# Kernel tuning notes

Hardware: AMD Instinct MI355X
Metric: run time of the kernel (lower is better)

The kernel has to match this reference:

```python
import jax, jax.numpy as jnp
import numpy as np
from jax import lax


def gru_cell(x, h, Wih, Whh, bih, bhh):
    # PyTorch GRU cell: gates ordered [r, z, n]
    gi = x @ Wih.T + bih            # [B, 3H]
    gh = h @ Whh.T + bhh            # [B, 3H]
    ir, iz, inn = jnp.split(gi, 3, axis=-1)
    hr, hz, hn = jnp.split(gh, 3, axis=-1)
    r = jax.nn.sigmoid(ir + hr)
    z = jax.nn.sigmoid(iz + hz)
    n = jnp.tanh(inn + r * hn)
    return (1.0 - z) * n + z * h


def setup_inputs() -> dict:
    key = jax.random.key(0)
    Vs = Vt = 32000; E = 256; H = 512; B = 32; S = 256; T = 64
    ks = jax.random.split(key, 32)

    def p(k, shape):
        return jax.random.normal(k, shape, dtype=jnp.float32) * 0.05

    return {
        "src": jax.random.randint(ks[0], (B, S), 0, Vs),
        "tgt": jax.random.randint(ks[1], (B, T), 0, Vt),
        "enc_emb": p(ks[2], (Vs, E)),
        "enc_Wih": p(ks[3], (3 * H, E)),
        "enc_Whh": p(ks[4], (3 * H, H)),
        "enc_bih": p(ks[5], (3 * H,)),
        "enc_bhh": p(ks[6], (3 * H,)),
        "dec_emb": p(ks[7], (Vt, E)),
        "attn_W1": p(ks[8], (H, H)),
        "attn_b1": p(ks[9], (H,)),
        "attn_W2": p(ks[10], (H, H)),
        "attn_b2": p(ks[11], (H,)),
        "attn_v": p(ks[12], (H,)),
        "dec_Wih": p(ks[13], (3 * H, E + H)),
        "dec_Whh": p(ks[14], (3 * H, H)),
        "dec_bih": p(ks[15], (3 * H,)),
        "dec_bhh": p(ks[16], (3 * H,)),
        "fc_W": p(ks[17], (Vt, H)),
        "fc_b": p(ks[18], (Vt,)),
    }


def reference(src, tgt, enc_emb, enc_Wih, enc_Whh, enc_bih, enc_bhh,
              dec_emb, attn_W1, attn_b1, attn_W2, attn_b2, attn_v,
              dec_Wih, dec_Whh, dec_bih, dec_bhh, fc_W, fc_b):
    B = src.shape[0]
    H = enc_Whh.shape[1]

    # ---- Encoder: GRU over src tokens ----
    src_e = enc_emb[src]                       # [B, S, E]

    def enc_step(h, x_t):
        h2 = gru_cell(x_t, h, enc_Wih, enc_Whh, enc_bih, enc_bhh)
        return h2, h2

    h0 = jnp.zeros((B, H), dtype=src_e.dtype)
    hT, enc_outs = lax.scan(enc_step, h0, src_e.transpose(1, 0, 2))
    enc_outs = enc_outs.transpose(1, 0, 2)     # [B, S, H]

    # Precompute encoder-side attention projection (loop-invariant)
    enc_proj = enc_outs @ attn_W2.T + attn_b2  # [B, S, H]

    # ---- Decoder: per-step Bahdanau attention + GRU + fc ----
    tgt_e = dec_emb[tgt].transpose(1, 0, 2)    # [T, B, E]

    def dec_step(h, x_t):
        q = jnp.tanh(enc_proj + (h @ attn_W1.T + attn_b1)[:, None, :])  # [B,S,H]
        scores = q @ attn_v                                             # [B,S]
        w = jax.nn.softmax(scores, axis=-1)
        ctx = jnp.einsum('bs,bsh->bh', w, enc_outs)                     # [B,H]
        rnn_in = jnp.concatenate([x_t, ctx], axis=-1)                   # [B,E+H]
        h2 = gru_cell(rnn_in, h, dec_Wih, dec_Whh, dec_bih, dec_bhh)
        logits = h2 @ fc_W.T + fc_b                                     # [B,V]
        return h2, logits

    _, outs = lax.scan(dec_step, hT, tgt_e)    # [T, B, V]
    return outs.transpose(1, 0, 2)             # [B, T, V]
```

## Files before the change

### kernel.cpp

```cpp
#include <hip/hip_runtime.h>
#include <hip/hip_bf16.h>
#include <stdint.h>

#define DEV __device__ __forceinline__
typedef unsigned short u16;
typedef unsigned int   u32;
typedef unsigned long long u64;

static constexpr int SS = 256;
static constexpr int TT = 64;
static constexpr int EE = 256;
static constexpr int HH = 512;
static constexpr int G3 = 1536;
static constexpr int VV = 32000;
static constexpr int HP  = 516;
static constexpr int WPE = 516;
static constexpr int WPD = 520;
static constexpr int CP8 = 520;

using frag   = __attribute__((ext_vector_type(8))) short;
using f32x4v = __attribute__((ext_vector_type(4))) float;

DEV float blo(u32 u){ union{u32 i; float f;} x; x.i = u << 16;         return x.f; }
DEV float bhi(u32 u){ union{u32 i; float f;} x; x.i = u & 0xffff0000u; return x.f; }
DEV float bf2f(u16 u){ union{u32 i; float f;} x; x.i = ((u32)u) << 16; return x.f; }
DEV u16 f2bf(float f){ union{float f; u32 u;} v; v.f = f;
  u32 r = v.u + 0x7fffu + ((v.u >> 16) & 1u); return (u16)(r >> 16); }
DEV float sigf (float x){ return 1.0f / (1.0f + __expf(-x)); }
DEV float tanh_(float x){ return 1.0f - 2.0f / (1.0f + __expf(2.0f * x)); }
DEV void unp8(float* d, uint4 u){
  d[0]=blo(u.x); d[1]=bhi(u.x); d[2]=blo(u.y); d[3]=bhi(u.y);
  d[4]=blo(u.z); d[5]=bhi(u.z); d[6]=blo(u.w); d[7]=bhi(u.w);
}
DEV float4 unp4(u64 v){
  return make_float4(bf2f((u16)v), bf2f((u16)(v >> 16)),
                     bf2f((u16)(v >> 32)), bf2f((u16)(v >> 48)));
}
DEV float dot4(float acc, float4 w, float4 x){
  acc = fmaf(w.x,x.x,acc); acc = fmaf(w.y,x.y,acc);
  acc = fmaf(w.z,x.z,acc); acc = fmaf(w.w,x.w,acc);
  return acc;
}
DEV float fma44(float acc, float4 w0, float4 w1, float4 h0, float4 h1){
  return dot4(dot4(acc, w0, h0), w1, h1);
}
DEV float fma8(float acc, const float* w, float4 a, float4 b){
  acc = fmaf(w[0],a.x,acc); acc = fmaf(w[1],a.y,acc);
  acc = fmaf(w[2],a.z,acc); acc = fmaf(w[3],a.w,acc);
  acc = fmaf(w[4],b.x,acc); acc = fmaf(w[5],b.y,acc);
  acc = fmaf(w[6],b.z,acc); acc = fmaf(w[7],b.w,acc);
  return acc;
}
DEV float fma8p(float acc, const float* w, const float* x){
  #pragma unroll
  for (int e = 0; e < 8; ++e) acc = fmaf(w[e], x[e], acc);
  return acc;
}

DEV void  ast_f(float* p, float v){ __hip_atomic_store(p, v, __ATOMIC_RELAXED, __HIP_MEMORY_SCOPE_AGENT); }
DEV void  ast_u(u32* p, u32 v)    { __hip_atomic_store(p, v, __ATOMIC_RELAXED, __HIP_MEMORY_SCOPE_AGENT); }
DEV float ald_f(const float* p)   { return __hip_atomic_load((float*)p, __ATOMIC_RELAXED, __HIP_MEMORY_SCOPE_AGENT); }
DEV u64   ald_u8(const u64* p)    { return __hip_atomic_load((u64*)p,   __ATOMIC_RELAXED, __HIP_MEMORY_SCOPE_AGENT); }
DEV u32   ald_u (const u32* p)    { return __hip_atomic_load((u32*)p,   __ATOMIC_RELAXED, __HIP_MEMORY_SCOPE_AGENT); }

DEV void grid_bar(u32* flags, int bid, int nb, u32 epoch){
  __syncthreads();
  if (threadIdx.x == 0) ast_u(&flags[bid * 32], epoch);
  if (threadIdx.x < (u32)nb) {
    while (ald_u(&flags[threadIdx.x * 32]) < epoch)
      __builtin_amdgcn_s_sleep(1);
  }
  __syncthreads();
}

__global__ __launch_bounds__(256)
void k_embed_gemm(const int* __restrict__ tok, int Tlen,
                  const float* __restrict__ emb,
                  const float* __restrict__ W, int wstride,
                  const float* __restrict__ bias,
                  u16* __restrict__ gi)
{
  __shared__ float es[16][EE];
  const int tid = threadIdx.x;
  const int r0 = blockIdx.y * 16;
  #pragma unroll
  for (int rr = 0; rr < 16; ++rr) {
    int r = r0 + rr;
    int token = tok[(r & 31) * Tlen + (r >> 5)];
    es[rr][tid] = emb[(size_t)token * EE + tid];
  }
  __syncthreads();
  const int jl = tid & 63;
  const int rg = (tid >> 6) << 2;
  const int jbase = blockIdx.x * 256 + jl;
  float acc[4][4];
  #pragma unroll
  for (int jj = 0; jj < 4; ++jj) {
    float bv = bias[jbase + jj * 64];
    #pragma unroll
    for (int rr = 0; rr < 4; ++rr) acc[jj][rr] = bv;
  }
  const float4* w0 = (const float4*)(W + (size_t)(jbase      ) * wstride);
  const float4* w1 = (const float4*)(W + (size_t)(jbase +  64) * wstride);
  const float4* w2 = (const float4*)(W + (size_t)(jbase + 128) * wstride);
  const float4* w3 = (const float4*)(W + (size_t)(jbase + 192) * wstride);
  for (int k4 = 0; k4 < EE / 4; ++k4) {
    float4 wv0 = w0[k4], wv1 = w1[k4], wv2 = w2[k4], wv3 = w3[k4];
    #pragma unroll
    for (int rr = 0; rr < 4; ++rr) {
      float4 e = *(const float4*)&es[rg + rr][k4 * 4];
      acc[0][rr] = dot4(acc[0][rr], wv0, e);
      acc[1][rr] = dot4(acc[1][rr], wv1, e);
      acc[2][rr] = dot4(acc[2][rr], wv2, e);
      acc[3][rr] = dot4(acc[3][rr], wv3, e);
    }
  }
  #pragma unroll
  for (int rr = 0; rr < 4; ++rr)
    #pragma unroll
    for (int jj = 0; jj < 4; ++jj)
      gi[(size_t)(r0 + rg + rr) * G3 + jbase + jj * 64] = f2bf(acc[jj][rr]);
}

__global__ __launch_bounds__(256)
void k_enc_scan(const u16* __restrict__ gi, const float* __restrict__ Whh,
                const float* __restrict__ bhh, u16* __restrict__ hring,
                u16* __restrict__ enc_outs, u32* __restrict__ flags)
{
  __shared__ float hs[32 * HP];
  __shared__ float wsl[12 * WPE];
  __shared__ float h2t[4][32];
  const int tid = threadIdx.x;
  const int bid = blockIdx.x;
  const int i0 = bid * 4;
  #pragma unroll
  for (int j = 0; j < 6; ++j) {
    int f = (j * 256 + tid) * 4;
    int rowl = f >> 9, k = f & 511;
    int g = rowl >> 2, ri = rowl & 3;
    *(float4*)&wsl[rowl * WPE + k] =
      *(const float4*)(Whh + (size_t)(g * 512 + i0 + ri) * 512 + k);
  }
  const int i_l = tid >> 6, lane = tid & 63, b = lane >> 1, kh = lane & 1;
  const int i = i0 + i_l;
  const float* w0 = wsl + (0 * 4 + i_l) * WPE + kh * 256;
  const float* w1 = wsl + (1 * 4 + i_l) * WPE + kh * 256;
  const float* w2 = wsl + (2 * 4 + i_l) * WPE + kh * 256;
  const float bR = bhh[i], bZ = bhh[i + 512], bN = bhh[i + 1024];
  for (int t = 0; t < SS; ++t) {
    const u64* hsrc = (const u64*)(hring + (size_t)t * 16384);
    #pragma unroll
    for (int j = 0; j < 16; ++j) {
      int idx = j * 256 + tid;
      u64 v = ald_u8(hsrc + idx);
      int bb = idx >> 7, m = (idx & 127) * 4;
      *(float4*)&hs[bb * HP + m] = unp4(v);
    }
    __syncthreads();
    float aR = 0.f, aZ = 0.f, aN = 0.f;
    const float* hb = hs + b * HP + kh * 256;
    for (int k8 = 0; k8 < 32; ++k8) {
      float4 h0 = *(const float4*)&hb[k8*8], h1 = *(const float4*)&hb[k8*8+4];
      aR = fma44(aR, *(const float4*)&w0[k8*8], *(const float4*)&w0[k8*8+4], h0, h1);
      aZ = fma44(aZ, *(const float4*)&w1[k8*8], *(const float4*)&w1[k8*8+4], h0, h1);
      aN = fma44(aN, *(const float4*)&w2[k8*8], *(const float4*)&w2[k8*8+4], h0, h1);
    }
    aR += __shfl_xor(aR, 1);
    aZ += __shfl_xor(aZ, 1);
    aN += __shfl_xor(aN, 1);
    if (kh == 0) {
      const size_t g = ((size_t)t * 32 + b) * G3;
      float r = sigf (bf2f(gi[g +        i]) + aR + bR);
      float z = sigf (bf2f(gi[g +  512 + i]) + aZ + bZ);
      float n = tanh_(bf2f(gi[g + 1024 + i]) + r * (aN + bN));
      float h2 = z * hs[b * HP + i] + (1.f - z) * n;
      enc_outs[((size_t)b * 256 + t) * 512 + i] = f2bf(h2);
      h2t[i_l][b] = h2;
    }
    __syncthreads();
    if (tid < 64) {
      int p = tid >> 5, bq = tid & 31;
      u32 pk = (u32)f2bf(h2t[2*p][bq]) | ((u32)f2bf(h2t[2*p+1][bq]) << 16);
      ast_u((u32*)(hring + (size_t)(t + 1) * 16384) + bq * 256 + bid * 2 + p, pk);
    }
    grid_bar(flags, bid, 128, (u32)(t + 1));
  }
}

__global__ __launch_bounds__(256)
void k_proj(const u16* __restrict__ A, const float* __restrict__ W,
            const float* __restrict__ bias, u16* __restrict__ Out)
{
  __shared__ float es[16][HH];
  const int tid = threadIdx.x;
  const int r0 = blockIdx.y * 16;
  #pragma unroll
  for (int j = 0; j < 4; ++j) {
    int u = j * 256 + tid;
    int row = u >> 6, k = (u & 63) * 8;
    float d[8]; unp8(d, *(const uint4*)(A + (size_t)(r0 + row) * HH + k));
    *(float4*)&es[row][k]     = make_float4(d[0],d[1],d[2],d[3]);
    *(float4*)&es[row][k + 4] = make_float4(d[4],d[5],d[6],d[7]);
  }
  __syncthreads();
  const int jl = tid & 63;
  const int rg = (tid >> 6) << 2;
  const int jbase = blockIdx.x * 256 + jl;
  float acc[4][4];
  #pragma unroll
  for (int jj = 0; jj < 4; ++jj) {
    float bv = bias[jbase + jj * 64];
    #pragma unroll
    for (int rr = 0; rr < 4; ++rr) acc[jj][rr] = bv;
  }
  const float4* w0 = (const float4*)(W + (size_t)(jbase      ) * HH);
  const float4* w1 = (const float4*)(W + (size_t)(jbase +  64) * HH);
  const float4* w2 = (const float4*)(W + (size_t)(jbase + 128) * HH);
  const float4* w3 = (const float4*)(W + (size_t)(jbase + 192) * HH);
  for (int k4 = 0; k4 < HH / 4; ++k4) {
    float4 wv0 = w0[k4], wv1 = w1[k4], wv2 = w2[k4], wv3 = w3[k4];
    #pragma unroll
    for (int rr = 0; rr < 4; ++rr) {
      float4 e = *(const float4*)&es[rg + rr][k4 * 4];
      acc[0][rr] = dot4(acc[0][rr], wv0, e);
      acc[1][rr] = dot4(acc[1][rr], wv1, e);
      acc[2][rr] = dot4(acc[2][rr], wv2, e);
      acc[3][rr] = dot4(acc[3][rr], wv3, e);
    }
  }
  #pragma unroll
  for (int rr = 0; rr < 4; ++rr)
    #pragma unroll
    for (int jj = 0; jj < 4; ++jj)
      Out[(size_t)(r0 + rg + rr) * HH + jbase + jj * 64] = f2bf(acc[jj][rr]);
}

__global__ __launch_bounds__(256)
void k_dec_scan(const u16* __restrict__ gi, u16* __restrict__ hring,
                const float* __restrict__ W1, const float* __restrict__ b1,
                const float* __restrict__ av,
                const u16* __restrict__ enc_proj, const u16* __restrict__ enc_outs,
                const float* __restrict__ Whh, const float* __restrict__ Wih,
                const float* __restrict__ bhh,
                float* __restrict__ aring, u16* __restrict__ ctxP,
                float* __restrict__ sringP, u16* __restrict__ h2bf,
                u32* __restrict__ flags)
{
  __shared__ float hs8[8 * HP];
  __shared__ u16  csb8[8 * CP8];
  __shared__ u16  wlds[112 * WPD];
  __shared__ float as_[512], vs_[512];
  __shared__ float scq[4][64], wts[64];
  __shared__ float rs[8];
  __shared__ float h2t[16][8];
  const int tid = threadIdx.x;
  const int bid = blockIdx.x;
  const int bg = bid >> 5, ig = bid & 31;
  const int b_l = tid >> 5, i_l = (tid >> 1) & 15, kh = tid & 1;
  const int i = ig * 16 + i_l;
  const int bglob = bg * 8 + b_l;
  const int pb = bid >> 2, sq = bid & 3;
  vs_[tid] = av[tid]; vs_[tid + 256] = av[tid + 256];
  for (int j = 0; j < 56; ++j) {
    int idx = j * 256 + tid;
    int row = idx >> 7, k4 = idx & 127;
    const float* src;
    if (row < 16)      src = W1  + (size_t)(ig * 16 + row) * 512 + k4 * 4;
    else if (row < 64) { int rr = row - 16; int g = rr >> 4, ii = rr & 15;
                         src = Whh + (size_t)(g * 512 + ig * 16 + ii) * 512 + k4 * 4; }
    else               { int rr = row - 64; int g = rr >> 4, ii = rr & 15;
                         src = Wih + (size_t)(g * 512 + ig * 16 + ii) * 768 + 256 + k4 * 4; }
    float4 w = *(const float4*)src;
    int f = row * WPD + k4 * 4;
    wlds[f] = f2bf(w.x); wlds[f+1] = f2bf(w.y); wlds[f+2] = f2bf(w.z); wlds[f+3] = f2bf(w.w);
  }
  const u16* w1r = wlds + (      i_l) * WPD + kh * 256;
  const u16* whr = wlds + (16  + i_l) * WPD + kh * 256;
  const u16* whz = wlds + (32  + i_l) * WPD + kh * 256;
  const u16* whn = wlds + (48  + i_l) * WPD + kh * 256;
  const u16* wir = wlds + (64  + i_l) * WPD + kh * 256;
  const u16* wiz = wlds + (80  + i_l) * WPD + kh * 256;
  const u16* win = wlds + (96  + i_l) * WPD + kh * 256;
  const float bR = bhh[i], bZ = bhh[i + 512], bN = bhh[i + 1024];
  const float b1i = b1[i];
  u32 ep = 0;
  for (int t = 0; t < TT; ++t) {
    const u64* hsrc = (const u64*)(hring + (size_t)(256 + t) * 16384);
    #pragma unroll
    for (int j = 0; j < 4; ++j) {
      int idx = j * 256 + tid;
      int lb = idx >> 7, gu = idx & 127;
      u64 v = ald_u8(hsrc + (size_t)(bg * 8 + lb) * 128 + gu);
      *(float4*)&hs8[lb * HP + gu * 4] = unp4(v);
    }
    __syncthreads();
    {
      const float* hb = hs8 + b_l * HP + kh * 256;
      float acc = 0.f;
      for (int k8 = 0; k8 < 32; ++k8) {
        float wf[8]; unp8(wf, *(const uint4*)(w1r + k8 * 8));
        acc = fma8(acc, wf, *(const float4*)&hb[k8*8], *(const float4*)&hb[k8*8+4]);
      }
      acc += __shfl_xor(acc, 1);
      if (kh == 0) ast_f(&aring[(size_t)t * 16384 + bglob * 512 + i], acc + b1i);
    }
    ++ep; grid_bar(flags, bid, 128, ep);
    {
      u64 v = ald_u8((const u64*)(aring + (size_t)t * 16384 + pb * 512) + tid);
      union { u64 q; float f[2]; } cv; cv.q = v;
      as_[2 * tid] = cv.f[0]; as_[2 * tid + 1] = cv.f[1];
    }
    __syncthreads();
    {
      const int kp = tid >> 6, s_l = tid & 63;
      const int s = sq * 64 + s_l;
      const u16* pr = enc_proj + ((size_t)pb * 256 + s) * 512 + kp * 128;
      const float* ak = as_ + kp * 128;
      const float* vk = vs_ + kp * 128;
      float acc = 0.f;
      for (int k8 = 0; k8 < 16; ++k8) {
        float d[8]; unp8(d, *(const uint4*)(pr + k8 * 8));
        #pragma unroll
        for (int e = 0; e < 8; ++e)
          acc += vk[k8 * 8 + e] * tanh_(d[e] + ak[k8 * 8 + e]);
      }
      scq[kp][s_l] = acc;
    }
    __syncthreads();
    if (tid < 64) {
      float sc = (scq[0][tid] + scq[1][tid]) + (scq[2][tid] + scq[3][tid]);
      float e = __expf(sc);
      wts[tid] = e;
      float su = e;
      #pragma unroll
      for (int d = 1; d < 64; d <<= 1) su += __shfl_xor(su, d);
      if (tid == 0) ast_f(&sringP[t * 128 + sq * 32 + pb], su);
    }
    __syncthreads();
    {
      const int k0 = tid * 2;
      float c0 = 0.f, c1 = 0.f;
      const u16* eo = enc_outs + ((size_t)pb * 256 + sq * 64) * 512 + k0;
      for (int s = 0; s < 64; ++s) {
        float w = wts[s];
        u32 pair = *(const u32*)(eo + (size_t)s * 512);
        c0 = fmaf(w, blo(pair), c0);
        c1 = fmaf(w, bhi(pair), c1);
      }
      u32 pk = (u32)f2bf(c0) | ((u32)f2bf(c1) << 16);
      ast_u((u32*)(ctxP + (size_t)t * 65536 + (sq * 32 + pb) * 512 + k0), pk);
    }
    ++ep; grid_bar(flags, bid, 128, ep);
    if (tid < 8) {
      const float* sp = sringP + t * 128;
      int bq = bg * 8 + tid;
      rs[tid] = 1.f / ((ald_f(sp + bq) + ald_f(sp + 32 + bq)) +
                       (ald_f(sp + 64 + bq) + ald_f(sp + 96 + bq)));
    }
    __syncthreads();
    #pragma unroll
    for (int j = 0; j < 4; ++j) {
      int idx = j * 256 + tid;
      int lb = idx >> 7, gu = idx & 127;
      const u64* bp = (const u64*)(ctxP + (size_t)t * 65536);
      float c[4] = {0,0,0,0};
      #pragma unroll
      for (int q = 0; q < 4; ++q) {
        float4 d = unp4(ald_u8(bp + (size_t)(q * 32 + bg * 8 + lb) * 128 + gu));
        c[0] += d.x; c[1] += d.y; c[2] += d.z; c[3] += d.w;
      }
      float r = rs[lb];
      int m = gu * 4;
      *(u32*)&csb8[lb * CP8 + m]     = (u32)f2bf(c[0]*r) | ((u32)f2bf(c[1]*r) << 16);
      *(u32*)&csb8[lb * CP8 + m + 2] = (u32)f2bf(c[2]*r) | ((u32)f2bf(c[3]*r) << 16);
    }
    __syncthreads();
    {
      const float* hb = hs8 + b_l * HP + kh * 256;
      const u16*   cb = csb8 + b_l * CP8 + kh * 256;
      float hR=0.f,hZ=0.f,hN=0.f,cR=0.f,cZ=0.f,cN=0.f;
      for (int k8 = 0; k8 < 32; ++k8) {
        float4 h0 = *(const float4*)&hb[k8*8], h1 = *(const float4*)&hb[k8*8+4];
        float cf[8]; unp8(cf, *(const uint4*)(cb + k8 * 8));
        float wf[8];
        unp8(wf, *(const uint4*)(whr + k8 * 8)); hR = fma8(hR, wf, h0, h1);
        unp8(wf, *(const uint4*)(whz + k8 * 8)); hZ = fma8(hZ, wf, h0, h1);
        unp8(wf, *(const uint4*)(whn + k8 * 8)); hN = fma8(hN, wf, h0, h1);
        unp8(wf, *(const uint4*)(wir + k8 * 8)); cR = fma8p(cR, wf, cf);
        unp8(wf, *(const uint4*)(wiz + k8 * 8)); cZ = fma8p(cZ, wf, cf);
        unp8(wf, *(const uint4*)(win + k8 * 8)); cN = fma8p(cN, wf, cf);
      }
      hR += __shfl_xor(hR, 1); hZ += __shfl_xor(hZ, 1); hN += __shfl_xor(hN, 1);
      cR += __shfl_xor(cR, 1); cZ += __shfl_xor(cZ, 1); cN += __shfl_xor(cN, 1);
      if (kh == 0) {
        const size_t g = ((size_t)t * 32 + bglob) * G3;
        float r = sigf (bf2f(gi[g +        i]) + cR + hR + bR);
        float z = sigf (bf2f(gi[g +  512 + i]) + cZ + hZ + bZ);
        float n = tanh_(bf2f(gi[g + 1024 + i]) + cN + r * (hN + bN));
        float h2 = z * hs8[b_l * HP + i] + (1.f - z) * n;
        h2bf[((size_t)t * 32 + bglob) * 512 + i] = f2bf(h2);
        h2t[i_l][b_l] = h2;
      }
    }
    __syncthreads();
    if (tid < 64) {
      int p = tid >> 3, bl = tid & 7;
      u32 pk = (u32)f2bf(h2t[2*p][bl]) | ((u32)f2bf(h2t[2*p+1][bl]) << 16);
      ast_u((u32*)(hring + (size_t)(257 + t) * 16384)
            + (bg * 8 + bl) * 256 + ig * 8 + p, pk);
    }
    ++ep; grid_bar(flags, bid, 128, ep);
  }
}

__global__ __launch_bounds__(256)
void k_cvt(const float* __restrict__ in, u16* __restrict__ out)
{
  size_t i = ((size_t)blockIdx.x * 256 + threadIdx.x) * 8;
  float4 a = *(const float4*)(in + i);
  float4 b = *(const float4*)(in + i + 4);
  union { uint4 v; u16 s[8]; } u;
  u.s[0]=f2bf(a.x); u.s[1]=f2bf(a.y); u.s[2]=f2bf(a.z); u.s[3]=f2bf(a.w);
  u.s[4]=f2bf(b.x); u.s[5]=f2bf(b.y); u.s[6]=f2bf(b.z); u.s[7]=f2bf(b.w);
  *(uint4*)(out + i) = u.v;
}

__global__ __launch_bounds__(256)
void k_logits_mfma(const u16* __restrict__ A, const u16* __restrict__ Wb,
                   const float* __restrict__ bias, float* __restrict__ out)
{
  __shared__ u16 Al[64 * 512];
  const int tid = threadIdx.x;
  const int r0 = blockIdx.x * 64;
  const int v0 = blockIdx.y * 64;
  {
    const uint4* src = (const uint4*)(A + (size_t)r0 * 512);
    uint4* dst = (uint4*)Al;
    #pragma unroll
    for (int j = 0; j < 16; ++j) {
      int idx = j * 256 + tid;
      int row = idx >> 6, g = idx & 63;
      dst[(row << 6) | (g ^ (row & 7))] = src[idx];
    }
  }
  const int w  = tid >> 6, l = tid & 63;
  const int lr = l & 15,  qk = l >> 4;
  const int v  = v0 + w * 16 + lr;
  frag bfr[16];
  {
    const u16* wrow = Wb + (size_t)v * 512 + qk * 8;
    #pragma unroll
    for (int ks = 0; ks < 16; ++ks)
      bfr[ks] = *(const frag*)(wrow + ks * 32);
  }
  const float bv = bias[v];
  __syncthreads();
  f32x4v acc[4];
  #pragma unroll
  for (int mt = 0; mt < 4; ++mt) acc[mt] = (f32x4v){0.f, 0.f, 0.f, 0.f};
  #pragma unroll
  for (int ks = 0; ks < 16; ++ks) {
    #pragma unroll
    for (int mt = 0; mt < 4; ++mt) {
      const int row = mt * 16 + lr;
      const int gr  = ks * 4 + qk;
      frag a = *(const frag*)&Al[(row << 9) | ((gr ^ (row & 7)) << 3)];
      acc[mt] = __builtin_amdgcn_mfma_f32_16x16x32_bf16(a, bfr[ks], acc[mt], 0, 0, 0);
    }
  }
  #pragma unroll
  for (int mt = 0; mt < 4; ++mt)
    #pragma unroll
    for (int reg = 0; reg < 4; ++reg) {
      const int r = r0 + mt * 16 + qk * 4 + reg;
      out[(size_t)(r & 31) * 64 * VV + (size_t)(r >> 5) * VV + v] = acc[mt][reg] + bv;
    }
}

extern "C" void kernel_launch(void* const* d_in, const int* in_sizes, int n_in,
                              void* d_out, int out_size, void* d_ws, size_t ws_size,
                              hipStream_t stream) {
  (void)in_sizes; (void)n_in; (void)out_size; (void)ws_size;
  const int*   src  = (const int*)d_in[0];
  const int*   tgt  = (const int*)d_in[1];
  const float* eemb = (const float*)d_in[2];
  const float* eWih = (const float*)d_in[3];
  const float* eWhh = (const float*)d_in[4];
  const float* ebih = (const float*)d_in[5];
  const float* ebhh = (const float*)d_in[6];
  const float* demb = (const float*)d_in[7];
  const float* aW1  = (const float*)d_in[8];
  const float* ab1  = (const float*)d_in[9];
  const float* aW2  = (const float*)d_in[10];
  const float* ab2  = (const float*)d_in[11];
  const float* av   = (const float*)d_in[12];
  const float* dWih = (const float*)d_in[13];
  const float* dWhh = (const float*)d_in[14];
  const float* dbih = (const float*)d_in[15];
  const float* dbhh = (const float*)d_in[16];
  const float* fcW  = (const float*)d_in[17];
  const float* fcb  = (const float*)d_in[18];
  float* out = (float*)d_out;

  float* aring   = (float*)d_ws;
  float* sringP  = aring + 1048576;
  u32*   flags   = (u32*)(sringP + 8192);
  u16*  ctxP     = (u16*)(flags + 8192);
  u16*  hring    = ctxP + 4194304;
  u16*  h2bf     = hring + 5259264;
  u16*  gi_enc   = h2bf + 1048576;
  u16*  gi_dec   = gi_enc + 12582912;
  u16*  enc_outs = gi_dec + 3145728;
  u16*  enc_proj = enc_outs + 4194304;
  u16*  wbf      = gi_enc;

  hipMemsetAsync(hring, 0, 16384 * sizeof(u16), stream);
  hipMemsetAsync(flags, 0, 8192 * sizeof(u32), stream);

  k_embed_gemm<<<dim3(6, 512), 256, 0, stream>>>(src, SS, eemb, eWih, EE,  ebih, gi_enc);
  k_embed_gemm<<<dim3(6, 128), 256, 0, stream>>>(tgt, TT, demb, dWih, 768, dbih, gi_dec);

  k_enc_scan<<<128, 256, 0, stream>>>(gi_enc, eWhh, ebhh, hring, enc_outs, flags);

  k_proj<<<dim3(2, 512), 256, 0, stream>>>(enc_outs, aW2, ab2, enc_proj);

  k_dec_scan<<<128, 256, 0, stream>>>(gi_dec, hring, aW1, ab1, av,
                                      enc_proj, enc_outs, dWhh, dWih, dbhh,
                                      aring, ctxP, sringP, h2bf, flags + 4096);

  k_cvt<<<8000, 256, 0, stream>>>(fcW, wbf);

  k_logits_mfma<<<dim3(32, 500), 256, 0, stream>>>(h2bf, wbf, fcb, out);
}
```

Measured before the change: 5.357 ms.

## Split encoder scan across batch halves using 256 persistent blocks

The encoder recurrent scan now runs on 256 blocks instead of 128. Each block handles 16 of the 32 batch rows for its 4 hidden units, and the K dimension is split four ways with a two-level shuffle reduction. Each block loads half as much hidden state per step and does half the FMAs, which shortens the serial per-step critical path. In exchange, each block still loads the full weight slice, the grid barrier now waits on twice as many blocks, and the flags region is enlarged and shifted to make room.

```diff
diff --git a/kernel.cpp b/kernel.cpp
--- a/kernel.cpp
+++ b/kernel.cpp
@@ -127,12 +127,13 @@
                 const float* __restrict__ bhh, u16* __restrict__ hring,
                 u16* __restrict__ enc_outs, u32* __restrict__ flags)
 {
-  __shared__ float hs[32 * HP];
+  __shared__ float hs16[16 * HP];
   __shared__ float wsl[12 * WPE];
-  __shared__ float h2t[4][32];
+  __shared__ float h2t[4][16];
   const int tid = threadIdx.x;
   const int bid = blockIdx.x;
-  const int i0 = bid * 4;
+  const int bh = bid >> 7, ig = bid & 127;
+  const int i0 = ig * 4, b0 = bh * 16;
   #pragma unroll
   for (int j = 0; j < 6; ++j) {
     int f = (j * 256 + tid) * 4;
@@ -141,49 +142,51 @@
     *(float4*)&wsl[rowl * WPE + k] =
       *(const float4*)(Whh + (size_t)(g * 512 + i0 + ri) * 512 + k);
   }
-  const int i_l = tid >> 6, lane = tid & 63, b = lane >> 1, kh = lane & 1;
+  const int i_l = tid >> 6, lane = tid & 63, b_l = lane >> 2, kq = lane & 3;
   const int i = i0 + i_l;
-  const float* w0 = wsl + (0 * 4 + i_l) * WPE + kh * 256;
-  const float* w1 = wsl + (1 * 4 + i_l) * WPE + kh * 256;
-  const float* w2 = wsl + (2 * 4 + i_l) * WPE + kh * 256;
+  const float* w0 = wsl + (0 * 4 + i_l) * WPE + kq * 128;
+  const float* w1 = wsl + (1 * 4 + i_l) * WPE + kq * 128;
+  const float* w2 = wsl + (2 * 4 + i_l) * WPE + kq * 128;
   const float bR = bhh[i], bZ = bhh[i + 512], bN = bhh[i + 1024];
   for (int t = 0; t < SS; ++t) {
     const u64* hsrc = (const u64*)(hring + (size_t)t * 16384);
     #pragma unroll
-    for (int j = 0; j < 16; ++j) {
+    for (int j = 0; j < 8; ++j) {
       int idx = j * 256 + tid;
-      u64 v = ald_u8(hsrc + idx);
-      int bb = idx >> 7, m = (idx & 127) * 4;
-      *(float4*)&hs[bb * HP + m] = unp4(v);
+      int lb = idx >> 7, gu = idx & 127;
+      u64 v = ald_u8(hsrc + (size_t)(b0 + lb) * 128 + gu);
+      *(float4*)&hs16[lb * HP + gu * 4] = unp4(v);
     }
     __syncthreads();
     float aR = 0.f, aZ = 0.f, aN = 0.f;
-    const float* hb = hs + b * HP + kh * 256;
-    for (int k8 = 0; k8 < 32; ++k8) {
+    const float* hb = hs16 + b_l * HP + kq * 128;
+    for (int k8 = 0; k8 < 16; ++k8) {
       float4 h0 = *(const float4*)&hb[k8*8], h1 = *(const float4*)&hb[k8*8+4];
       aR = fma44(aR, *(const float4*)&w0[k8*8], *(const float4*)&w0[k8*8+4], h0, h1);
       aZ = fma44(aZ, *(const float4*)&w1[k8*8], *(const float4*)&w1[k8*8+4], h0, h1);
       aN = fma44(aN, *(const float4*)&w2[k8*8], *(const float4*)&w2[k8*8+4], h0, h1);
     }
-    aR += __shfl_xor(aR, 1);
-    aZ += __shfl_xor(aZ, 1);
-    aN += __shfl_xor(aN, 1);
-    if (kh == 0) {
-      const size_t g = ((size_t)t * 32 + b) * G3;
+    aR += __shfl_xor(aR, 1); aR += __shfl_xor(aR, 2);
+    aZ += __shfl_xor(aZ, 1); aZ += __shfl_xor(aZ, 2);
+    aN += __shfl_xor(aN, 1); aN += __shfl_xor(aN, 2);
+    if (kq == 0) {
+      const int bg = b0 + b_l;
+      const size_t g = ((size_t)t * 32 + bg) * G3;
       float r = sigf (bf2f(gi[g +        i]) + aR + bR);
       float z = sigf (bf2f(gi[g +  512 + i]) + aZ + bZ);
       float n = tanh_(bf2f(gi[g + 1024 + i]) + r * (aN + bN));
-      float h2 = z * hs[b * HP + i] + (1.f - z) * n;
-      enc_outs[((size_t)b * 256 + t) * 512 + i] = f2bf(h2);
-      h2t[i_l][b] = h2;
-    }
-    __syncthreads();
-    if (tid < 64) {
-      int p = tid >> 5, bq = tid & 31;
-      u32 pk = (u32)f2bf(h2t[2*p][bq]) | ((u32)f2bf(h2t[2*p+1][bq]) << 16);
-      ast_u((u32*)(hring + (size_t)(t + 1) * 16384) + bq * 256 + bid * 2 + p, pk);
-    }
-    grid_bar(flags, bid, 128, (u32)(t + 1));
+      float h2 = z * hs16[b_l * HP + i] + (1.f - z) * n;
+      enc_outs[((size_t)bg * 256 + t) * 512 + i] = f2bf(h2);
+      h2t[i_l][b_l] = h2;
+    }
+    __syncthreads();
+    if (tid < 32) {
+      int p = tid >> 4, bl = tid & 15;
+      u32 pk = (u32)f2bf(h2t[2*p][bl]) | ((u32)f2bf(h2t[2*p+1][bl]) << 16);
+      ast_u((u32*)(hring + (size_t)(t + 1) * 16384)
+            + (b0 + bl) * 256 + (i0 >> 1) + p, pk);
+    }
+    grid_bar(flags, bid, 256, (u32)(t + 1));
   }
 }
 
@@ -505,7 +508,7 @@
   float* aring   = (float*)d_ws;
   float* sringP  = aring + 1048576;
   u32*   flags   = (u32*)(sringP + 8192);
-  u16*  ctxP     = (u16*)(flags + 8192);
+  u16*  ctxP     = (u16*)(flags + 12288);
   u16*  hring    = ctxP + 4194304;
   u16*  h2bf     = hring + 5259264;
   u16*  gi_enc   = h2bf + 1048576;
@@ -515,18 +518,18 @@
   u16*  wbf      = gi_enc;
 
   hipMemsetAsync(hring, 0, 16384 * sizeof(u16), stream);
-  hipMemsetAsync(flags, 0, 8192 * sizeof(u32), stream);
+  hipMemsetAsync(flags, 0, 12288 * sizeof(u32), stream);
 
   k_embed_gemm<<<dim3(6, 512), 256, 0, stream>>>(src, SS, eemb, eWih, EE,  ebih, gi_enc);
   k_embed_gemm<<<dim3(6, 128), 256, 0, stream>>>(tgt, TT, demb, dWih, 768, dbih, gi_dec);
 
-  k_enc_scan<<<128, 256, 0, stream>>>(gi_enc, eWhh, ebhh, hring, enc_outs, flags);
+  k_enc_scan<<<256, 256, 0, stream>>>(gi_enc, eWhh, ebhh, hring, enc_outs, flags);
 
   k_proj<<<dim3(2, 512), 256, 0, stream>>>(enc_outs, aW2, ab2, enc_proj);
 
   k_dec_scan<<<128, 256, 0, stream>>>(gi_dec, hring, aW1, ab1, av,
                                       enc_proj, enc_outs, dWhh, dWih, dbhh,
-                                      aring, ctxP, sringP, h2bf, flags + 4096);
+                                      aring, ctxP, sringP, h2bf, flags + 8192);
 
   k_cvt<<<8000, 256, 0, stream>>>(fcW, wbf);
 
```

Result: faster. 4.948 ms, median of 3 (-7.6%).
